# Kernel optimization log

Measured on AMD Instinct MI355X. Metric: run time of the kernel, lower is better.

Reference implementation:

```python
import jax, jax.numpy as jnp
import numpy as np

N_NODES = 20000
N_EDGES = 160000
MUL0, MUL1 = 32, 16          # 32x0e + 16x1o for both in and out irreps
EDGE_FEAT = 128
HIDDEN = 128
W_SIZES = [MUL0*MUL0, MUL1*MUL0, MUL0*MUL1, MUL1*MUL1, MUL1*MUL1]  # uvw weights per path (sh muls are 1)
W_OFF = np.cumsum([0] + W_SIZES).tolist()
W_NUMEL = W_OFF[-1]          # 2560
EPS_LN = 1e-5

_e = np.zeros((3, 3, 3), np.float32)
for i, j, k in [(0, 1, 2), (1, 2, 0), (2, 0, 1)]:
    _e[i, j, k] = 1.0
    _e[i, k, j] = -1.0
EPS3 = jnp.asarray(_e)  # Levi-Civita for 1o x 1o -> 1o path


def setup_inputs() -> dict:
    key = jax.random.key(0)
    ks = jax.random.split(key, 8)
    node_attr = jax.random.normal(ks[0], (N_NODES, MUL0 + 3 * MUL1), jnp.float32)
    edge_index = jax.random.randint(ks[1], (2, N_EDGES), 0, N_NODES)
    edge_attr = jax.random.normal(ks[2], (N_EDGES, EDGE_FEAT), jnp.float32)
    edge_sh = jax.random.normal(ks[3], (N_EDGES, 4), jnp.float32)
    s1 = float(1.0 / np.sqrt(EDGE_FEAT))
    s2 = float(1.0 / np.sqrt(HIDDEN))
    fc_w1 = jax.random.uniform(ks[4], (EDGE_FEAT, HIDDEN), jnp.float32, -s1, s1)
    fc_b1 = jnp.zeros((HIDDEN,), jnp.float32)
    fc_w2 = jax.random.uniform(ks[5], (HIDDEN, W_NUMEL), jnp.float32, -s2, s2)
    fc_b2 = jnp.zeros((W_NUMEL,), jnp.float32)
    # LayerNorm params: mean_shift is ones for scalar (0e) irreps, zeros for 1o
    mean_shift = jnp.concatenate(
        [jnp.ones((1, MUL0, 1), jnp.float32), jnp.zeros((1, MUL1, 1), jnp.float32)], axis=1)
    affine_weight = jnp.ones((MUL0 + MUL1,), jnp.float32) + 0.1 * jax.random.normal(ks[6], (MUL0 + MUL1,), jnp.float32)
    affine_bias = 0.02 * jax.random.normal(ks[7], (MUL0,), jnp.float32)
    return dict(node_attr=node_attr, edge_attr=edge_attr, edge_sh=edge_sh,
                fc_w1=fc_w1, fc_b1=fc_b1, fc_w2=fc_w2, fc_b2=fc_b2,
                mean_shift=mean_shift, affine_weight=affine_weight,
                affine_bias=affine_bias, edge_index=edge_index)


def _forward(node_attr, edge_attr, edge_sh, fc_w1, fc_b1, fc_w2, fc_b2,
             mean_shift, affine_weight, affine_bias, edge_index):
    edge_src, edge_dst = edge_index[0], edge_index[1]
    # gather source-of-message node features per edge
    x = node_attr[edge_dst]                          # [E, 80]
    x0 = x[:, :MUL0]                                 # [E, 32]   l=0 scalars
    x1 = x[:, MUL0:].reshape(-1, MUL1, 3)            # [E, 16, 3] l=1 vectors
    sh0 = edge_sh[:, 0]                              # [E]
    sh1 = edge_sh[:, 1:4]                            # [E, 3]

    # per-edge TP weights from edge features (SimpleLinear: Lin-ReLU-Lin, dropout=0)
    w = jnp.maximum(edge_attr @ fc_w1 + fc_b1, 0.0) @ fc_w2 + fc_b2   # [E, 2560]
    w1 = w[:, W_OFF[0]:W_OFF[1]].reshape(-1, MUL0, MUL0)
    w2 = w[:, W_OFF[1]:W_OFF[2]].reshape(-1, MUL1, MUL0)
    w3 = w[:, W_OFF[2]:W_OFF[3]].reshape(-1, MUL0, MUL1)
    w4 = w[:, W_OFF[3]:W_OFF[4]].reshape(-1, MUL1, MUL1)
    w5 = w[:, W_OFF[4]:W_OFF[5]].reshape(-1, MUL1, MUL1)

    # e3nn FullyConnectedTensorProduct normalization (component + element):
    # coeff = sqrt(ir_out.dim / sum_of_fan_in_over_paths_to_that_output)
    c0 = float(np.sqrt(1.0 / (MUL0 + MUL1)))            # -> 0e: fan 32+16
    c1 = float(np.sqrt(3.0 / (MUL0 + MUL1 + MUL1)))     # -> 1o: fan 32+16+16
    is3 = float(1.0 / np.sqrt(3.0))  # wigner-3j (110),(011),(101)
    is6 = float(1.0 / np.sqrt(6.0))  # wigner-3j (111)

    out0 = c0 * (jnp.einsum('eu,e,euw->ew', x0, sh0, w1)
                 + is3 * jnp.einsum('eui,ei,euw->ew', x1, sh1, w2))            # [E, 32]
    out1 = c1 * (is3 * jnp.einsum('eu,ek,euw->ewk', x0, sh1, w3)
                 + is3 * jnp.einsum('eui,e,euw->ewi', x1, sh0, w4)
                 + is6 * jnp.einsum('ijk,eui,ej,euw->ewk', EPS3, x1, sh1, w5)) # [E, 16, 3]
    tp = jnp.concatenate([out0, out1.reshape(-1, MUL1 * 3)], axis=-1)          # [E, 80]

    # scatter-mean over destination (edge_src) nodes
    seg = jax.ops.segment_sum(tp, edge_src, num_segments=N_NODES)
    cnt = jax.ops.segment_sum(jnp.ones((tp.shape[0],), tp.dtype), edge_src, num_segments=N_NODES)
    out = seg / jnp.maximum(cnt, 1.0)[:, None]

    # residual (out irreps == in irreps, so F.pad is a no-op)
    out = out + node_attr

    # equivariant LayerNorm (normalization='component')
    f0 = out[:, :MUL0].reshape(-1, MUL0, 1)
    f0 = f0 - jnp.mean(f0, axis=1, keepdims=True) * mean_shift[:, :MUL0]
    n0 = jnp.mean(jnp.mean(f0 * f0, axis=-1), axis=1, keepdims=True)           # [N, 1]
    n0 = jax.lax.rsqrt(n0 + EPS_LN) * affine_weight[None, :MUL0]               # [N, 32]
    f0 = f0 * n0[:, :, None] + affine_bias[None, :, None]

    f1 = out[:, MUL0:].reshape(-1, MUL1, 3)
    f1 = f1 - jnp.mean(f1, axis=1, keepdims=True) * mean_shift[:, MUL0:]       # mean_shift=0 here
    n1 = jnp.mean(jnp.mean(f1 * f1, axis=-1), axis=1, keepdims=True)
    n1 = jax.lax.rsqrt(n1 + EPS_LN) * affine_weight[None, MUL0:]
    f1 = f1 * n1[:, :, None]

    return jnp.concatenate([f0.reshape(-1, MUL0), f1.reshape(-1, MUL1 * 3)], axis=-1)


def reference(node_attr, edge_attr, edge_sh, fc_w1, fc_b1, fc_w2, fc_b2,
              mean_shift, affine_weight, affine_bias, edge_index):
    return _forward(node_attr, edge_attr, edge_sh, fc_w1, fc_b1, fc_w2, fc_b2,
                    mean_shift, affine_weight, affine_bias, edge_index)
```

## Files before the change

### kernel.cpp

```cpp
#include <hip/hip_runtime.h>

typedef __attribute__((ext_vector_type(8))) short short8;
typedef __attribute__((ext_vector_type(4))) short bfx4;
typedef __attribute__((ext_vector_type(4))) float floatx4;

#define N_NODES 20000
#define N_EDGES 160000
#define TILE_E 128
#define EBLK (N_EDGES / TILE_E)

#define C0f   0.14433756729740643f
#define C1f   0.21650635094610965f
#define IS3   0.5773502691896258f
#define IS6   0.4082482904638631f
#define EPS_LN 1e-5f

#define W1F_OFF 0
#define W2F_OFF 32768
#define CNT_OFF 688128

__device__ __forceinline__ short f2bf(float f) {
    unsigned u = __float_as_uint(f);
    u += 0x7fff + ((u >> 16) & 1);
    return (short)(u >> 16);
}
__device__ __forceinline__ float bf2f(short s) {
    return __uint_as_float(((unsigned)(unsigned short)s) << 16);
}

__device__ __forceinline__ short8 load8_bf16(const float* p) {
    const float4* q = (const float4*)p;
    float4 f0 = q[0], f1 = q[1];
    short8 s;
    s[0]=f2bf(f0.x); s[1]=f2bf(f0.y); s[2]=f2bf(f0.z); s[3]=f2bf(f0.w);
    s[4]=f2bf(f1.x); s[5]=f2bf(f1.y); s[6]=f2bf(f1.z); s[7]=f2bf(f1.w);
    return s;
}

__device__ __forceinline__ floatx4 mfma4(const short8* a, short8 b0, short8 b1,
                                         short8 b2, short8 b3, float bias) {
    floatx4 C = {bias, bias, bias, bias};
    C = __builtin_amdgcn_mfma_f32_16x16x32_bf16(a[0], b0, C, 0, 0, 0);
    C = __builtin_amdgcn_mfma_f32_16x16x32_bf16(a[1], b1, C, 0, 0, 0);
    C = __builtin_amdgcn_mfma_f32_16x16x32_bf16(a[2], b2, C, 0, 0, 0);
    C = __builtin_amdgcn_mfma_f32_16x16x32_bf16(a[3], b3, C, 0, 0, 0);
    return C;
}

__device__ __forceinline__ int xsw(int row, int el) {
    return row * 64 + ((el & 3) | ((((el >> 2) ^ row) & 15) << 2));
}
__device__ __forceinline__ bfx4 ldx(const short* base, int row, int gran) {
    return *(const bfx4*)(base + row * 64 + (((gran ^ row) & 15) << 2));
}

__global__ __launch_bounds__(256)
void prep_kernel(const float* __restrict__ fc_w1, const float* __restrict__ fc_w2,
                 short* __restrict__ w1f, short* __restrict__ w2f,
                 float* __restrict__ cnt) {
    int g = blockIdx.x * 256 + threadIdx.x;
    if (g < N_NODES) cnt[g] = 0.0f;
    if (g < 2048) {
        int ln = g & 15, qd = (g >> 4) & 3, kt = (g >> 6) & 3, t = g >> 8;
        int n = t * 16 + ln, kb = kt * 32 + qd * 8;
        short8 s;
        #pragma unroll
        for (int j = 0; j < 8; ++j) s[j] = f2bf(fc_w1[(kb + j) * 128 + n]);
        *(short8*)(w1f + g * 8) = s;
        return;
    }
    int g2 = g - 2048;
    if (g2 < 40960) {
        int ln = g2 & 15, qd = (g2 >> 4) & 3, kt = (g2 >> 6) & 3, t = g2 >> 8;
        int n = t * 16 + ln, kb = kt * 32 + qd * 8;
        short8 s;
        #pragma unroll
        for (int j = 0; j < 8; ++j) s[j] = f2bf(fc_w2[(kb + j) * 2560 + n]);
        int p = (t < 128) ? t : (t < 144 ? 128 + 2 * (t - 128) : 129 + 2 * (t - 144));
        *(short8*)(w2f + (size_t)p * 2048 + (g2 & 255) * 8) = s;
    }
}

__global__ __launch_bounds__(256, 2)
void edge_kernel(const float* __restrict__ node_attr,
                 const float* __restrict__ edge_attr,
                 const float* __restrict__ edge_sh,
                 const float* __restrict__ fc_b1,
                 const float* __restrict__ fc_b2,
                 const int*   __restrict__ edge_index,
                 const short* __restrict__ w1f,
                 const short* __restrict__ w2f,
                 float* __restrict__ accum,
                 float* __restrict__ cnt)
{
    __shared__ __align__(16) short s_pool[128 * 136];
    __shared__ __align__(16) short s_w2[2 * 8192];
    __shared__ float s_sh[128 * 4];
    __shared__ int   s_src[128];
    __shared__ int   s_dst[128];

    short* s_H    = s_pool;
    short* s_x0t  = s_pool;
    short* s_x1t  = s_pool + 4096;
    short* s_x1dt = s_pool + 10240;

    const int tid  = threadIdx.x;
    const int e0   = blockIdx.x * TILE_E;
    const int lane = tid & 63;
    const int wv   = tid >> 6;

    float4 st0, st1, st2, st3;
    {
        const float4* sp = (const float4*)w2f;
        st0 = sp[tid]; st1 = sp[tid + 256]; st2 = sp[tid + 512]; st3 = sp[tid + 768];
    }

    if (tid < 128) {
        int s = edge_index[e0 + tid];
        int d = edge_index[N_EDGES + e0 + tid];
        s_src[tid] = s; s_dst[tid] = d;
        atomicAdd(&cnt[s], 1.0f);
    }
    s_sh[tid]       = edge_sh[(size_t)e0 * 4 + tid];
    s_sh[tid + 256] = edge_sh[(size_t)e0 * 4 + tid + 256];
    __syncthreads();

    const int ln   = lane & 15;
    const int qd   = lane >> 4;
    const int eb0  = wv * 32 + qd * 4;
    const int eb1  = eb0 + 16;
    const int half = wv >> 1;
    const int gr0  = (wv & 1) * 8 + qd;
    const int gr1  = gr0 + 4;
    const short* x0b  = s_x0t  + half * 2048;
    const short* x1b  = s_x1t  + half * 3072;
    const short* x1db = s_x1dt + half * 1024;

    {
        short8 a1[2][4];
        #pragma unroll
        for (int g = 0; g < 2; ++g) {
            const float* ap = edge_attr + (size_t)(e0 + wv*32 + g*16 + ln) * 128 + qd * 8;
            #pragma unroll
            for (int kt = 0; kt < 4; ++kt) a1[g][kt] = load8_bf16(ap + kt * 32);
        }
        #pragma unroll
        for (int t = 0; t < 8; ++t) {
            const short* bp = w1f + t * 2048 + lane * 8;
            short8 b0 = *(const short8*)bp;
            short8 b1 = *(const short8*)(bp + 512);
            short8 b2 = *(const short8*)(bp + 1024);
            short8 b3 = *(const short8*)(bp + 1536);
            float bias = fc_b1[t * 16 + ln];
            #pragma unroll
            for (int g = 0; g < 2; ++g) {
                floatx4 C = mfma4(a1[g], b0, b1, b2, b3, bias);
                #pragma unroll
                for (int r = 0; r < 4; ++r)
                    s_H[(wv*32 + g*16 + qd*4 + r) * 136 + t*16 + ln] = f2bf(fmaxf(C[r], 0.f));
            }
        }
    }

    short8 a2[2][4];
    #pragma unroll
    for (int g = 0; g < 2; ++g) {
        const short* hp = s_H + (wv*32 + g*16 + ln) * 136 + qd * 8;
        #pragma unroll
        for (int kt = 0; kt < 4; ++kt) a2[g][kt] = *(const short8*)(hp + kt * 32);
    }
    __syncthreads();

    #pragma unroll
    for (int i = 0; i < 40; ++i) {
        int f = tid + i * 256;
        int e = f / 80, c = f % 80;
        float v = node_attr[(size_t)s_dst[e] * 80 + c];
        int hf = e >> 6, el = e & 63;
        if (c < 32) s_x0t[hf * 2048 + xsw(c, el)] = f2bf(v);
        else        s_x1t[hf * 3072 + xsw(c - 32, el)] = f2bf(v);
    }
    #pragma unroll
    for (int i = 0; i < 8; ++i) {
        int it = tid + i * 256;
        int e = it >> 4, u = it & 15;
        const float* xp = node_attr + (size_t)s_dst[e] * 80 + 32 + u * 3;
        float d = xp[0] * s_sh[e*4+1] + xp[1] * s_sh[e*4+2] + xp[2] * s_sh[e*4+3];
        s_x1dt[(e >> 6) * 1024 + xsw(u, e & 63)] = f2bf(d);
    }
    __syncthreads();

    {
        float4* dp = (float4*)s_w2;
        dp[tid] = st0; dp[tid+256] = st1; dp[tid+512] = st2; dp[tid+768] = st3;
        const float4* sp = (const float4*)(w2f + (size_t)8192);
        st0 = sp[tid]; st1 = sp[tid+256]; st2 = sp[tid+512]; st3 = sp[tid+768];
    }
    __syncthreads();


    float r0lo[2][4] = {}, r0hi[2][4] = {}, r1lo[2][4] = {}, r1hi[2][4] = {};

    #pragma unroll 1
    for (int c = 0; c < 16; ++c) {
        {
            float4* dp = (float4*)(s_w2 + ((c + 1) & 1) * 8192);
            dp[tid] = st0; dp[tid+256] = st1; dp[tid+512] = st2; dp[tid+768] = st3;
            const float4* sp = (const float4*)(w2f + (size_t)(c + 2) * 8192);
            st0 = sp[tid]; st1 = sp[tid+256]; st2 = sp[tid+512]; st3 = sp[tid+768];
        }
        const short* bb = s_w2 + (c & 1) * 8192 + lane * 8;
        #pragma unroll
        for (int t = 0; t < 2; ++t) {
            const int u = 2 * c + t;
            const short* bp = bb + t * 4096;
            short8 L0 = *(const short8*)bp,          L1 = *(const short8*)(bp + 512);
            short8 L2 = *(const short8*)(bp + 1024), L3 = *(const short8*)(bp + 1536);
            short8 H0 = *(const short8*)(bp + 2048), H1 = *(const short8*)(bp + 2560);
            short8 H2 = *(const short8*)(bp + 3072), H3 = *(const short8*)(bp + 3584);
            float blo = fc_b2[u * 32 + ln], bhi = fc_b2[u * 32 + 16 + ln];
            #pragma unroll
            for (int g = 0; g < 2; ++g) {
                floatx4 Clo = mfma4(a2[g], L0, L1, L2, L3, blo);
                floatx4 Chi = mfma4(a2[g], H0, H1, H2, H3, bhi);
                bfx4 xs = ldx(x0b, u, g ? gr1 : gr0);
                #pragma unroll
                for (int r = 0; r < 4; ++r) {
                    float a = bf2f(xs[r]);
                    r0lo[g][r] += a * Clo[r];
                    r0hi[g][r] += a * Chi[r];
                }
            }
        }
        __syncthreads();
    }
    #pragma unroll 1
    for (int c2 = 0; c2 < 8; ++c2) {
        const int c = 16 + c2;
        {
            float4* dp = (float4*)(s_w2 + ((c + 1) & 1) * 8192);
            dp[tid] = st0; dp[tid+256] = st1; dp[tid+512] = st2; dp[tid+768] = st3;
            const float4* sp = (const float4*)(w2f + (size_t)(c + 2) * 8192);
            st0 = sp[tid]; st1 = sp[tid+256]; st2 = sp[tid+512]; st3 = sp[tid+768];
        }
        const short* bb = s_w2 + (c & 1) * 8192 + lane * 8;
        #pragma unroll
        for (int t = 0; t < 2; ++t) {
            const int u = 2 * c2 + t;
            const short* bp = bb + t * 4096;
            short8 L0 = *(const short8*)bp,          L1 = *(const short8*)(bp + 512);
            short8 L2 = *(const short8*)(bp + 1024), L3 = *(const short8*)(bp + 1536);
            short8 H0 = *(const short8*)(bp + 2048), H1 = *(const short8*)(bp + 2560);
            short8 H2 = *(const short8*)(bp + 3072), H3 = *(const short8*)(bp + 3584);
            float blo = fc_b2[1024 + u * 32 + ln], bhi = fc_b2[1024 + u * 32 + 16 + ln];
            #pragma unroll
            for (int g = 0; g < 2; ++g) {
                floatx4 Clo = mfma4(a2[g], L0, L1, L2, L3, blo);
                floatx4 Chi = mfma4(a2[g], H0, H1, H2, H3, bhi);
                bfx4 xs = ldx(x1db, u, g ? gr1 : gr0);
                #pragma unroll
                for (int r = 0; r < 4; ++r) {
                    float a = bf2f(xs[r]);
                    r1lo[g][r] += a * Clo[r];
                    r1hi[g][r] += a * Chi[r];
                }
            }
        }
        __syncthreads();
    }
    #pragma unroll
    for (int g = 0; g < 2; ++g)
        #pragma unroll
        for (int r = 0; r < 4; ++r) {
            int e = (g ? eb1 : eb0) + r;
            float sh0 = s_sh[e*4];
            int base = s_src[e] * 80;
            atomicAdd(&accum[base + ln],      C0f * (sh0 * r0lo[g][r] + IS3 * r1lo[g][r]));
            atomicAdd(&accum[base + 16 + ln], C0f * (sh0 * r0hi[g][r] + IS3 * r1hi[g][r]));
        }

    float r3[2][4] = {};
    float r4[2][4][3] = {};
    float r5[2][4][3] = {};

    #pragma unroll 1
    for (int c3 = 0; c3 < 8; ++c3) {
        const int c = 24 + c3;
        {
            float4* dp = (float4*)(s_w2 + ((c + 1) & 1) * 8192);
            dp[tid] = st0; dp[tid+256] = st1; dp[tid+512] = st2; dp[tid+768] = st3;
            const float4* sp = (const float4*)(w2f + (size_t)(c + 2) * 8192);
            st0 = sp[tid]; st1 = sp[tid+256]; st2 = sp[tid+512]; st3 = sp[tid+768];
        }
        const short* bb = s_w2 + (c & 1) * 8192 + lane * 8;
        #pragma unroll
        for (int t = 0; t < 4; ++t) {
            const int u = 4 * c3 + t;
            const short* bp = bb + t * 2048;
            short8 b0 = *(const short8*)bp,          b1 = *(const short8*)(bp + 512);
            short8 b2 = *(const short8*)(bp + 1024), b3 = *(const short8*)(bp + 1536);
            float bias = fc_b2[1536 + u * 16 + ln];
            #pragma unroll
            for (int g = 0; g < 2; ++g) {
                floatx4 C = mfma4(a2[g], b0, b1, b2, b3, bias);
                bfx4 xs = ldx(x0b, u, g ? gr1 : gr0);
                #pragma unroll
                for (int r = 0; r < 4; ++r)
                    r3[g][r] += bf2f(xs[r]) * C[r];
            }
        }
        __syncthreads();
    }
    #pragma unroll 1
    for (int c4 = 0; c4 < 8; ++c4) {
        const int c = 32 + c4;
        if (c4 < 7) {
            float4* dp = (float4*)(s_w2 + ((c + 1) & 1) * 8192);
            dp[tid] = st0; dp[tid+256] = st1; dp[tid+512] = st2; dp[tid+768] = st3;
            if (c4 < 6) {
                const float4* sp = (const float4*)(w2f + (size_t)(c + 2) * 8192);
                st0 = sp[tid]; st1 = sp[tid+256]; st2 = sp[tid+512]; st3 = sp[tid+768];
            }
        }
        const short* bb = s_w2 + (c & 1) * 8192 + lane * 8;
        #pragma unroll
        for (int t = 0; t < 2; ++t) {
            const int u = 2 * c4 + t;
            const short* bpF = bb + (2 * t) * 2048;
            short8 F0 = *(const short8*)bpF,          F1 = *(const short8*)(bpF + 512);
            short8 F2 = *(const short8*)(bpF + 1024), F3 = *(const short8*)(bpF + 1536);
            short8 G0 = *(const short8*)(bpF + 2048), G1 = *(const short8*)(bpF + 2560);
            short8 G2 = *(const short8*)(bpF + 3072), G3 = *(const short8*)(bpF + 3584);
            float b4 = fc_b2[2048 + u * 16 + ln], b5 = fc_b2[2304 + u * 16 + ln];
            #pragma unroll
            for (int g = 0; g < 2; ++g) {
                floatx4 C4 = mfma4(a2[g], F0, F1, F2, F3, b4);
                floatx4 C5 = mfma4(a2[g], G0, G1, G2, G3, b5);
                int gr = (g ? gr1 : gr0);
                bfx4 x0s = ldx(x1b, u*3 + 0, gr);
                bfx4 x1s = ldx(x1b, u*3 + 1, gr);
                bfx4 x2s = ldx(x1b, u*3 + 2, gr);
                #pragma unroll
                for (int r = 0; r < 4; ++r) {
                    float a0 = bf2f(x0s[r]), a1 = bf2f(x1s[r]), a2v = bf2f(x2s[r]);
                    r4[g][r][0] += a0 * C4[r];  r5[g][r][0] += a0 * C5[r];
                    r4[g][r][1] += a1 * C4[r];  r5[g][r][1] += a1 * C5[r];
                    r4[g][r][2] += a2v * C4[r]; r5[g][r][2] += a2v * C5[r];
                }
            }
        }
        if (c4 < 7) __syncthreads();
    }
    #pragma unroll
    for (int g = 0; g < 2; ++g)
        #pragma unroll
        for (int r = 0; r < 4; ++r) {
            int e = (g ? eb1 : eb0) + r;
            float sh0 = s_sh[e*4], sa = s_sh[e*4+1], sb = s_sh[e*4+2], sc = s_sh[e*4+3];
            int base = s_src[e] * 80;
            float t3 = C1f * IS3 * r3[g][r];
            float s0 = C1f * IS3 * sh0;
            float c6 = C1f * IS6;
            float v50 = r5[g][r][1] * sc - r5[g][r][2] * sb;
            float v51 = r5[g][r][2] * sa - r5[g][r][0] * sc;
            float v52 = r5[g][r][0] * sb - r5[g][r][1] * sa;
            atomicAdd(&accum[base + 32 + ln*3 + 0], sa * t3 + s0 * r4[g][r][0] + c6 * v50);
            atomicAdd(&accum[base + 32 + ln*3 + 1], sb * t3 + s0 * r4[g][r][1] + c6 * v51);
            atomicAdd(&accum[base + 32 + ln*3 + 2], sc * t3 + s0 * r4[g][r][2] + c6 * v52);
        }
}

__global__ __launch_bounds__(256)
void node_kernel(const float* __restrict__ node_attr,
                 const float* __restrict__ mean_shift,
                 const float* __restrict__ aw,
                 const float* __restrict__ ab,
                 const float* __restrict__ cnt,
                 float* __restrict__ out)
{
    __shared__ float sv[64 * 85];
    __shared__ float s_inv[64];
    const int tid = threadIdx.x;
    const int n0  = blockIdx.x * 64;

    if (tid < 64) {
        int n = n0 + tid;
        s_inv[tid] = (n < N_NODES) ? 1.0f / fmaxf(cnt[n], 1.0f) : 0.0f;
    }
    __syncthreads();

    #pragma unroll
    for (int i = 0; i < 20; ++i) {
        int idx = tid + i * 256;
        int r = idx / 80, cch = idx % 80;
        int n = n0 + r;
        if (n < N_NODES) {
            float o = out[(size_t)n * 80 + cch];
            float a = node_attr[(size_t)n * 80 + cch];
            sv[r * 85 + cch] = o * s_inv[r] + a;
        }
    }
    __syncthreads();

    if (tid < 64 && n0 + tid < N_NODES) {
        float v[80];
        const float* sp = sv + tid * 85;
        #pragma unroll
        for (int k = 0; k < 80; ++k) v[k] = sp[k];

        float m0 = 0.f;
        #pragma unroll
        for (int u = 0; u < 32; ++u) m0 += v[u];
        m0 *= (1.0f / 32.0f);
        float n0v = 0.f;
        #pragma unroll
        for (int u = 0; u < 32; ++u) {
            float f = v[u] - m0 * mean_shift[u];
            v[u] = f;
            n0v += f * f;
        }
        n0v = rsqrtf(n0v * (1.0f / 32.0f) + EPS_LN);
        #pragma unroll
        for (int u = 0; u < 32; ++u) v[u] = v[u] * (n0v * aw[u]) + ab[u];

        float m1[3] = {0.f, 0.f, 0.f};
        #pragma unroll
        for (int u = 0; u < 16; ++u)
            #pragma unroll
            for (int i = 0; i < 3; ++i) m1[i] += v[32 + u*3 + i];
        #pragma unroll
        for (int i = 0; i < 3; ++i) m1[i] *= (1.0f / 16.0f);
        float n1 = 0.f;
        #pragma unroll
        for (int u = 0; u < 16; ++u)
            #pragma unroll
            for (int i = 0; i < 3; ++i) {
                float f = v[32 + u*3 + i] - m1[i] * mean_shift[32 + u];
                v[32 + u*3 + i] = f;
                n1 += f * f;
            }
        n1 = rsqrtf(n1 * (1.0f / 48.0f) + EPS_LN);
        #pragma unroll
        for (int u = 0; u < 16; ++u)
            #pragma unroll
            for (int i = 0; i < 3; ++i)
                v[32 + u*3 + i] *= (n1 * aw[32 + u]);

        float* wp = sv + tid * 85;
        #pragma unroll
        for (int k = 0; k < 80; ++k) wp[k] = v[k];
    }
    __syncthreads();

    #pragma unroll
    for (int i = 0; i < 20; ++i) {
        int idx = tid + i * 256;
        int r = idx / 80, cch = idx % 80;
        int n = n0 + r;
        if (n < N_NODES) out[(size_t)n * 80 + cch] = sv[r * 85 + cch];
    }
}

extern "C" void kernel_launch(void* const* d_in, const int* in_sizes, int n_in,
                              void* d_out, int out_size, void* d_ws, size_t ws_size,
                              hipStream_t stream) {
    const float* node_attr  = (const float*)d_in[0];
    const float* edge_attr  = (const float*)d_in[1];
    const float* edge_sh    = (const float*)d_in[2];
    const float* fc_w1      = (const float*)d_in[3];
    const float* fc_b1      = (const float*)d_in[4];
    const float* fc_w2      = (const float*)d_in[5];
    const float* fc_b2      = (const float*)d_in[6];
    const float* mean_shift = (const float*)d_in[7];
    const float* aw         = (const float*)d_in[8];
    const float* ab         = (const float*)d_in[9];
    const int*   edge_index = (const int*)d_in[10];
    float* out = (float*)d_out;

    short* w1f = (short*)((char*)d_ws + W1F_OFF);
    short* w2f = (short*)((char*)d_ws + W2F_OFF);
    float* cnt = (float*)((char*)d_ws + CNT_OFF);

    (void)hipMemsetAsync(d_out, 0, (size_t)N_NODES * 80 * sizeof(float), stream);

    prep_kernel<<<(2048 + 40960 + 255) / 256, 256, 0, stream>>>(fc_w1, fc_w2, w1f, w2f, cnt);
    edge_kernel<<<EBLK, 256, 0, stream>>>(node_attr, edge_attr, edge_sh,
                                          fc_b1, fc_b2, edge_index,
                                          w1f, w2f, out, cnt);
    node_kernel<<<(N_NODES + 63) / 64, 256, 0, stream>>>(node_attr, mean_shift,
                                                         aw, ab, cnt, out);
}
```

Measured before the change: 336.4 us.

## Halve W2 staging chunks, swizzle hidden tile, fold output memset into prep

The double-buffered W2 staging now uses 8 KB chunks (80 steps) instead of 16 KB (40 steps). This halves the staging registers and the LDS W2 buffer. The hidden-activation tile drops its padding and uses an XOR swizzle to avoid bank conflicts, which shrinks LDS further. This is likely aimed at fitting more blocks per CU or easing register pressure. The output zeroing moves from a separate memset into the prep kernel, removing one launch, at the cost of twice as many block barriers in the edge kernel.

```diff
diff --git a/kernel.cpp b/kernel.cpp
--- a/kernel.cpp
+++ b/kernel.cpp
@@ -54,12 +54,18 @@
     return *(const bfx4*)(base + row * 64 + (((gran ^ row) & 15) << 2));
 }
 
+__device__ __forceinline__ int hsw(int row, int col) {
+    return row * 128 + (col & 7) + ((((col >> 3) ^ (row & 15)) & 15) << 3);
+}
+
 __global__ __launch_bounds__(256)
 void prep_kernel(const float* __restrict__ fc_w1, const float* __restrict__ fc_w2,
                  short* __restrict__ w1f, short* __restrict__ w2f,
-                 float* __restrict__ cnt) {
+                 float* __restrict__ cnt, float* __restrict__ out) {
     int g = blockIdx.x * 256 + threadIdx.x;
     if (g < N_NODES) cnt[g] = 0.0f;
+    float4 z = {0.f, 0.f, 0.f, 0.f};
+    for (int i = g; i < 400000; i += 43008) ((float4*)out)[i] = z;
     if (g < 2048) {
         int ln = g & 15, qd = (g >> 4) & 3, kt = (g >> 6) & 3, t = g >> 8;
         int n = t * 16 + ln, kb = kt * 32 + qd * 8;
@@ -67,17 +73,17 @@
         #pragma unroll
         for (int j = 0; j < 8; ++j) s[j] = f2bf(fc_w1[(kb + j) * 128 + n]);
         *(short8*)(w1f + g * 8) = s;
-        return;
-    }
-    int g2 = g - 2048;
-    if (g2 < 40960) {
-        int ln = g2 & 15, qd = (g2 >> 4) & 3, kt = (g2 >> 6) & 3, t = g2 >> 8;
-        int n = t * 16 + ln, kb = kt * 32 + qd * 8;
-        short8 s;
-        #pragma unroll
-        for (int j = 0; j < 8; ++j) s[j] = f2bf(fc_w2[(kb + j) * 2560 + n]);
-        int p = (t < 128) ? t : (t < 144 ? 128 + 2 * (t - 128) : 129 + 2 * (t - 144));
-        *(short8*)(w2f + (size_t)p * 2048 + (g2 & 255) * 8) = s;
+    } else {
+        int g2 = g - 2048;
+        if (g2 < 40960) {
+            int ln = g2 & 15, qd = (g2 >> 4) & 3, kt = (g2 >> 6) & 3, t = g2 >> 8;
+            int n = t * 16 + ln, kb = kt * 32 + qd * 8;
+            short8 s;
+            #pragma unroll
+            for (int j = 0; j < 8; ++j) s[j] = f2bf(fc_w2[(kb + j) * 2560 + n]);
+            int p = (t < 128) ? t : (t < 144 ? 128 + 2 * (t - 128) : 129 + 2 * (t - 144));
+            *(short8*)(w2f + (size_t)p * 2048 + (g2 & 255) * 8) = s;
+        }
     }
 }
 
@@ -93,8 +99,8 @@
                  float* __restrict__ accum,
                  float* __restrict__ cnt)
 {
-    __shared__ __align__(16) short s_pool[128 * 136];
-    __shared__ __align__(16) short s_w2[2 * 8192];
+    __shared__ __align__(16) short s_pool[128 * 128];
+    __shared__ __align__(16) short s_w2[2 * 4096];
     __shared__ float s_sh[128 * 4];
     __shared__ int   s_src[128];
     __shared__ int   s_dst[128];
@@ -109,10 +115,10 @@
     const int lane = tid & 63;
     const int wv   = tid >> 6;
 
-    float4 st0, st1, st2, st3;
+    float4 stA, stB;
     {
         const float4* sp = (const float4*)w2f;
-        st0 = sp[tid]; st1 = sp[tid + 256]; st2 = sp[tid + 512]; st3 = sp[tid + 768];
+        stA = sp[tid]; stB = sp[tid + 256];
     }
 
     if (tid < 128) {
@@ -157,7 +163,7 @@
                 floatx4 C = mfma4(a1[g], b0, b1, b2, b3, bias);
                 #pragma unroll
                 for (int r = 0; r < 4; ++r)
-                    s_H[(wv*32 + g*16 + qd*4 + r) * 136 + t*16 + ln] = f2bf(fmaxf(C[r], 0.f));
+                    s_H[hsw(wv*32 + g*16 + qd*4 + r, t*16 + ln)] = f2bf(fmaxf(C[r], 0.f));
             }
         }
     }
@@ -165,9 +171,11 @@
     short8 a2[2][4];
     #pragma unroll
     for (int g = 0; g < 2; ++g) {
-        const short* hp = s_H + (wv*32 + g*16 + ln) * 136 + qd * 8;
-        #pragma unroll
-        for (int kt = 0; kt < 4; ++kt) a2[g][kt] = *(const short8*)(hp + kt * 32);
+        const int row = wv*32 + g*16 + ln;
+        #pragma unroll
+        for (int kt = 0; kt < 4; ++kt)
+            a2[g][kt] = *(const short8*)(s_H + row * 128 +
+                                         (((qd + 4*kt) ^ (row & 15)) << 3));
     }
     __syncthreads();
 
@@ -188,82 +196,69 @@
         float d = xp[0] * s_sh[e*4+1] + xp[1] * s_sh[e*4+2] + xp[2] * s_sh[e*4+3];
         s_x1dt[(e >> 6) * 1024 + xsw(u, e & 63)] = f2bf(d);
     }
-    __syncthreads();
-
     {
         float4* dp = (float4*)s_w2;
-        dp[tid] = st0; dp[tid+256] = st1; dp[tid+512] = st2; dp[tid+768] = st3;
-        const float4* sp = (const float4*)(w2f + (size_t)8192);
-        st0 = sp[tid]; st1 = sp[tid+256]; st2 = sp[tid+512]; st3 = sp[tid+768];
-    }
-    __syncthreads();
-
+        dp[tid] = stA; dp[tid + 256] = stB;
+        const float4* sp = (const float4*)(w2f + 4096);
+        stA = sp[tid]; stB = sp[tid + 256];
+    }
+    __syncthreads();
+
+    auto stage_step = [&](int cg) {
+        if (cg + 1 < 80) {
+            float4* dp = (float4*)(s_w2 + ((cg + 1) & 1) * 4096);
+            dp[tid] = stA; dp[tid + 256] = stB;
+        }
+        if (cg + 2 < 80) {
+            const float4* sp = (const float4*)(w2f + (size_t)(cg + 2) * 4096);
+            stA = sp[tid]; stB = sp[tid + 256];
+        }
+    };
 
     float r0lo[2][4] = {}, r0hi[2][4] = {}, r1lo[2][4] = {}, r1hi[2][4] = {};
 
     #pragma unroll 1
-    for (int c = 0; c < 16; ++c) {
-        {
-            float4* dp = (float4*)(s_w2 + ((c + 1) & 1) * 8192);
-            dp[tid] = st0; dp[tid+256] = st1; dp[tid+512] = st2; dp[tid+768] = st3;
-            const float4* sp = (const float4*)(w2f + (size_t)(c + 2) * 8192);
-            st0 = sp[tid]; st1 = sp[tid+256]; st2 = sp[tid+512]; st3 = sp[tid+768];
-        }
-        const short* bb = s_w2 + (c & 1) * 8192 + lane * 8;
-        #pragma unroll
-        for (int t = 0; t < 2; ++t) {
-            const int u = 2 * c + t;
-            const short* bp = bb + t * 4096;
-            short8 L0 = *(const short8*)bp,          L1 = *(const short8*)(bp + 512);
-            short8 L2 = *(const short8*)(bp + 1024), L3 = *(const short8*)(bp + 1536);
-            short8 H0 = *(const short8*)(bp + 2048), H1 = *(const short8*)(bp + 2560);
-            short8 H2 = *(const short8*)(bp + 3072), H3 = *(const short8*)(bp + 3584);
-            float blo = fc_b2[u * 32 + ln], bhi = fc_b2[u * 32 + 16 + ln];
-            #pragma unroll
-            for (int g = 0; g < 2; ++g) {
-                floatx4 Clo = mfma4(a2[g], L0, L1, L2, L3, blo);
-                floatx4 Chi = mfma4(a2[g], H0, H1, H2, H3, bhi);
-                bfx4 xs = ldx(x0b, u, g ? gr1 : gr0);
-                #pragma unroll
-                for (int r = 0; r < 4; ++r) {
-                    float a = bf2f(xs[r]);
-                    r0lo[g][r] += a * Clo[r];
-                    r0hi[g][r] += a * Chi[r];
-                }
+    for (int c = 0; c < 32; ++c) {
+        stage_step(c);
+        const short* bp = s_w2 + (c & 1) * 4096 + lane * 8;
+        short8 L0 = *(const short8*)bp,          L1 = *(const short8*)(bp + 512);
+        short8 L2 = *(const short8*)(bp + 1024), L3 = *(const short8*)(bp + 1536);
+        short8 H0 = *(const short8*)(bp + 2048), H1 = *(const short8*)(bp + 2560);
+        short8 H2 = *(const short8*)(bp + 3072), H3 = *(const short8*)(bp + 3584);
+        float blo = fc_b2[c * 32 + ln], bhi = fc_b2[c * 32 + 16 + ln];
+        #pragma unroll
+        for (int g = 0; g < 2; ++g) {
+            floatx4 Clo = mfma4(a2[g], L0, L1, L2, L3, blo);
+            floatx4 Chi = mfma4(a2[g], H0, H1, H2, H3, bhi);
+            bfx4 xs = ldx(x0b, c, g ? gr1 : gr0);
+            #pragma unroll
+            for (int r = 0; r < 4; ++r) {
+                float a = bf2f(xs[r]);
+                r0lo[g][r] += a * Clo[r];
+                r0hi[g][r] += a * Chi[r];
             }
         }
         __syncthreads();
     }
     #pragma unroll 1
-    for (int c2 = 0; c2 < 8; ++c2) {
-        const int c = 16 + c2;
-        {
-            float4* dp = (float4*)(s_w2 + ((c + 1) & 1) * 8192);
-            dp[tid] = st0; dp[tid+256] = st1; dp[tid+512] = st2; dp[tid+768] = st3;
-            const float4* sp = (const float4*)(w2f + (size_t)(c + 2) * 8192);
-            st0 = sp[tid]; st1 = sp[tid+256]; st2 = sp[tid+512]; st3 = sp[tid+768];
-        }
-        const short* bb = s_w2 + (c & 1) * 8192 + lane * 8;
-        #pragma unroll
-        for (int t = 0; t < 2; ++t) {
-            const int u = 2 * c2 + t;
-            const short* bp = bb + t * 4096;
-            short8 L0 = *(const short8*)bp,          L1 = *(const short8*)(bp + 512);
-            short8 L2 = *(const short8*)(bp + 1024), L3 = *(const short8*)(bp + 1536);
-            short8 H0 = *(const short8*)(bp + 2048), H1 = *(const short8*)(bp + 2560);
-            short8 H2 = *(const short8*)(bp + 3072), H3 = *(const short8*)(bp + 3584);
-            float blo = fc_b2[1024 + u * 32 + ln], bhi = fc_b2[1024 + u * 32 + 16 + ln];
-            #pragma unroll
-            for (int g = 0; g < 2; ++g) {
-                floatx4 Clo = mfma4(a2[g], L0, L1, L2, L3, blo);
-                floatx4 Chi = mfma4(a2[g], H0, H1, H2, H3, bhi);
-                bfx4 xs = ldx(x1db, u, g ? gr1 : gr0);
-                #pragma unroll
-                for (int r = 0; r < 4; ++r) {
-                    float a = bf2f(xs[r]);
-                    r1lo[g][r] += a * Clo[r];
-                    r1hi[g][r] += a * Chi[r];
-                }
+    for (int c2 = 0; c2 < 16; ++c2) {
+        stage_step(32 + c2);
+        const short* bp = s_w2 + ((32 + c2) & 1) * 4096 + lane * 8;
+        short8 L0 = *(const short8*)bp,          L1 = *(const short8*)(bp + 512);
+        short8 L2 = *(const short8*)(bp + 1024), L3 = *(const short8*)(bp + 1536);
+        short8 H0 = *(const short8*)(bp + 2048), H1 = *(const short8*)(bp + 2560);
+        short8 H2 = *(const short8*)(bp + 3072), H3 = *(const short8*)(bp + 3584);
+        float blo = fc_b2[1024 + c2 * 32 + ln], bhi = fc_b2[1024 + c2 * 32 + 16 + ln];
+        #pragma unroll
+        for (int g = 0; g < 2; ++g) {
+            floatx4 Clo = mfma4(a2[g], L0, L1, L2, L3, blo);
+            floatx4 Chi = mfma4(a2[g], H0, H1, H2, H3, bhi);
+            bfx4 xs = ldx(x1db, c2, g ? gr1 : gr0);
+            #pragma unroll
+            for (int r = 0; r < 4; ++r) {
+                float a = bf2f(xs[r]);
+                r1lo[g][r] += a * Clo[r];
+                r1hi[g][r] += a * Chi[r];
             }
         }
         __syncthreads();
@@ -284,18 +279,12 @@
     float r5[2][4][3] = {};
 
     #pragma unroll 1
-    for (int c3 = 0; c3 < 8; ++c3) {
-        const int c = 24 + c3;
-        {
-            float4* dp = (float4*)(s_w2 + ((c + 1) & 1) * 8192);
-            dp[tid] = st0; dp[tid+256] = st1; dp[tid+512] = st2; dp[tid+768] = st3;
-            const float4* sp = (const float4*)(w2f + (size_t)(c + 2) * 8192);
-            st0 = sp[tid]; st1 = sp[tid+256]; st2 = sp[tid+512]; st3 = sp[tid+768];
-        }
-        const short* bb = s_w2 + (c & 1) * 8192 + lane * 8;
-        #pragma unroll
-        for (int t = 0; t < 4; ++t) {
-            const int u = 4 * c3 + t;
+    for (int c3 = 0; c3 < 16; ++c3) {
+        stage_step(48 + c3);
+        const short* bb = s_w2 + ((48 + c3) & 1) * 4096 + lane * 8;
+        #pragma unroll
+        for (int t = 0; t < 2; ++t) {
+            const int u = 2 * c3 + t;
             const short* bp = bb + t * 2048;
             short8 b0 = *(const short8*)bp,          b1 = *(const short8*)(bp + 512);
             short8 b2 = *(const short8*)(bp + 1024), b3 = *(const short8*)(bp + 1536);
@@ -312,44 +301,32 @@
         __syncthreads();
     }
     #pragma unroll 1
-    for (int c4 = 0; c4 < 8; ++c4) {
-        const int c = 32 + c4;
-        if (c4 < 7) {
-            float4* dp = (float4*)(s_w2 + ((c + 1) & 1) * 8192);
-            dp[tid] = st0; dp[tid+256] = st1; dp[tid+512] = st2; dp[tid+768] = st3;
-            if (c4 < 6) {
-                const float4* sp = (const float4*)(w2f + (size_t)(c + 2) * 8192);
-                st0 = sp[tid]; st1 = sp[tid+256]; st2 = sp[tid+512]; st3 = sp[tid+768];
-            }
-        }
-        const short* bb = s_w2 + (c & 1) * 8192 + lane * 8;
-        #pragma unroll
-        for (int t = 0; t < 2; ++t) {
-            const int u = 2 * c4 + t;
-            const short* bpF = bb + (2 * t) * 2048;
-            short8 F0 = *(const short8*)bpF,          F1 = *(const short8*)(bpF + 512);
-            short8 F2 = *(const short8*)(bpF + 1024), F3 = *(const short8*)(bpF + 1536);
-            short8 G0 = *(const short8*)(bpF + 2048), G1 = *(const short8*)(bpF + 2560);
-            short8 G2 = *(const short8*)(bpF + 3072), G3 = *(const short8*)(bpF + 3584);
-            float b4 = fc_b2[2048 + u * 16 + ln], b5 = fc_b2[2304 + u * 16 + ln];
-            #pragma unroll
-            for (int g = 0; g < 2; ++g) {
-                floatx4 C4 = mfma4(a2[g], F0, F1, F2, F3, b4);
-                floatx4 C5 = mfma4(a2[g], G0, G1, G2, G3, b5);
-                int gr = (g ? gr1 : gr0);
-                bfx4 x0s = ldx(x1b, u*3 + 0, gr);
-                bfx4 x1s = ldx(x1b, u*3 + 1, gr);
-                bfx4 x2s = ldx(x1b, u*3 + 2, gr);
-                #pragma unroll
-                for (int r = 0; r < 4; ++r) {
-                    float a0 = bf2f(x0s[r]), a1 = bf2f(x1s[r]), a2v = bf2f(x2s[r]);
-                    r4[g][r][0] += a0 * C4[r];  r5[g][r][0] += a0 * C5[r];
-                    r4[g][r][1] += a1 * C4[r];  r5[g][r][1] += a1 * C5[r];
-                    r4[g][r][2] += a2v * C4[r]; r5[g][r][2] += a2v * C5[r];
-                }
-            }
-        }
-        if (c4 < 7) __syncthreads();
+    for (int c4 = 0; c4 < 16; ++c4) {
+        const int cg = 64 + c4;
+        stage_step(cg);
+        const short* bb = s_w2 + (cg & 1) * 4096 + lane * 8;
+        short8 F0 = *(const short8*)bb,          F1 = *(const short8*)(bb + 512);
+        short8 F2 = *(const short8*)(bb + 1024), F3 = *(const short8*)(bb + 1536);
+        short8 G0 = *(const short8*)(bb + 2048), G1 = *(const short8*)(bb + 2560);
+        short8 G2 = *(const short8*)(bb + 3072), G3 = *(const short8*)(bb + 3584);
+        float b4 = fc_b2[2048 + c4 * 16 + ln], b5 = fc_b2[2304 + c4 * 16 + ln];
+        #pragma unroll
+        for (int g = 0; g < 2; ++g) {
+            floatx4 C4 = mfma4(a2[g], F0, F1, F2, F3, b4);
+            floatx4 C5 = mfma4(a2[g], G0, G1, G2, G3, b5);
+            int gr = (g ? gr1 : gr0);
+            bfx4 x0s = ldx(x1b, c4*3 + 0, gr);
+            bfx4 x1s = ldx(x1b, c4*3 + 1, gr);
+            bfx4 x2s = ldx(x1b, c4*3 + 2, gr);
+            #pragma unroll
+            for (int r = 0; r < 4; ++r) {
+                float a0 = bf2f(x0s[r]), a1 = bf2f(x1s[r]), a2v = bf2f(x2s[r]);
+                r4[g][r][0] += a0 * C4[r];  r5[g][r][0] += a0 * C5[r];
+                r4[g][r][1] += a1 * C4[r];  r5[g][r][1] += a1 * C5[r];
+                r4[g][r][2] += a2v * C4[r]; r5[g][r][2] += a2v * C5[r];
+            }
+        }
+        if (c4 < 15) __syncthreads();
     }
     #pragma unroll
     for (int g = 0; g < 2; ++g)
@@ -481,9 +458,8 @@
     short* w2f = (short*)((char*)d_ws + W2F_OFF);
     float* cnt = (float*)((char*)d_ws + CNT_OFF);
 
-    (void)hipMemsetAsync(d_out, 0, (size_t)N_NODES * 80 * sizeof(float), stream);
-
-    prep_kernel<<<(2048 + 40960 + 255) / 256, 256, 0, stream>>>(fc_w1, fc_w2, w1f, w2f, cnt);
+    prep_kernel<<<(2048 + 40960 + 255) / 256, 256, 0, stream>>>(fc_w1, fc_w2, w1f, w2f,
+                                                                cnt, out);
     edge_kernel<<<EBLK, 256, 0, stream>>>(node_attr, edge_attr, edge_sh,
                                           fc_b1, fc_b2, edge_index,
                                           w1f, w2f, out, cnt);
```

Measured after the change: 363.3 us. 1.08x slower.

## Replace float atomic scatter with CSR-bucketed per-edge writes and node-side gather

Applied to the files above, without the earlier changes.

Source-node degrees are counted in the prep kernel, then a single-block scan kernel builds per-node offsets. Each edge claims a slot with one integer atomic and writes its 80 message values to a slot-ordered buffer with plain stores instead of 80 float atomics. The node kernel then sums each node's contiguous slots before LayerNorm, which removes the memset of the output. This trades atomic contention for an extra ~51MB write and read pass, a serial single-block scan, and a workspace requirement that is not checked.

```diff
diff --git a/kernel.cpp b/kernel.cpp
--- a/kernel.cpp
+++ b/kernel.cpp
@@ -15,9 +15,13 @@
 #define IS6   0.4082482904638631f
 #define EPS_LN 1e-5f
 
-#define W1F_OFF 0
-#define W2F_OFF 32768
-#define CNT_OFF 688128
+#define W1F_OFF  0
+#define W2F_OFF  32768
+#define CNT_OFF  688128
+#define OFF_OFF  768128
+#define FILL_OFF 848128
+#define TP_OFF   1048576
+#define WS_NEED  (TP_OFF + (size_t)N_EDGES * 80 * 4)
 
 __device__ __forceinline__ short f2bf(float f) {
     unsigned u = __float_as_uint(f);
@@ -57,9 +61,13 @@
 __global__ __launch_bounds__(256)
 void prep_kernel(const float* __restrict__ fc_w1, const float* __restrict__ fc_w2,
                  short* __restrict__ w1f, short* __restrict__ w2f,
-                 float* __restrict__ cnt) {
+                 int* __restrict__ cnt, const int* __restrict__ edge_index,
+                 int do_count) {
     int g = blockIdx.x * 256 + threadIdx.x;
-    if (g < N_NODES) cnt[g] = 0.0f;
+    if (do_count) {
+        for (int e = g; e < N_EDGES; e += 43008)
+            atomicAdd(&cnt[edge_index[e]], 1);
+    }
     if (g < 2048) {
         int ln = g & 15, qd = (g >> 4) & 3, kt = (g >> 6) & 3, t = g >> 8;
         int n = t * 16 + ln, kb = kt * 32 + qd * 8;
@@ -67,17 +75,48 @@
         #pragma unroll
         for (int j = 0; j < 8; ++j) s[j] = f2bf(fc_w1[(kb + j) * 128 + n]);
         *(short8*)(w1f + g * 8) = s;
-        return;
-    }
-    int g2 = g - 2048;
-    if (g2 < 40960) {
-        int ln = g2 & 15, qd = (g2 >> 4) & 3, kt = (g2 >> 6) & 3, t = g2 >> 8;
-        int n = t * 16 + ln, kb = kt * 32 + qd * 8;
-        short8 s;
-        #pragma unroll
-        for (int j = 0; j < 8; ++j) s[j] = f2bf(fc_w2[(kb + j) * 2560 + n]);
-        int p = (t < 128) ? t : (t < 144 ? 128 + 2 * (t - 128) : 129 + 2 * (t - 144));
-        *(short8*)(w2f + (size_t)p * 2048 + (g2 & 255) * 8) = s;
+    } else {
+        int g2 = g - 2048;
+        if (g2 < 40960) {
+            int ln = g2 & 15, qd = (g2 >> 4) & 3, kt = (g2 >> 6) & 3, t = g2 >> 8;
+            int n = t * 16 + ln, kb = kt * 32 + qd * 8;
+            short8 s;
+            #pragma unroll
+            for (int j = 0; j < 8; ++j) s[j] = f2bf(fc_w2[(kb + j) * 2560 + n]);
+            int p = (t < 128) ? t : (t < 144 ? 128 + 2 * (t - 128) : 129 + 2 * (t - 144));
+            *(short8*)(w2f + (size_t)p * 2048 + (g2 & 255) * 8) = s;
+        }
+    }
+}
+
+__global__ __launch_bounds__(1024)
+void scan_kernel(const int* __restrict__ cnt, int* __restrict__ off,
+                 int* __restrict__ fill) {
+    __shared__ int part[1024];
+    const int t = threadIdx.x;
+    const int base = t * 20;
+    int loc[20];
+    int s = 0;
+    if (base < N_NODES) {
+        #pragma unroll
+        for (int i = 0; i < 20; ++i) { loc[i] = s; s += cnt[base + i]; }
+    }
+    part[t] = s;
+    __syncthreads();
+    for (int d = 1; d < 1024; d <<= 1) {
+        int v = (t >= d) ? part[t - d] : 0;
+        __syncthreads();
+        part[t] += v;
+        __syncthreads();
+    }
+    int pre = (t == 0) ? 0 : part[t - 1];
+    if (base < N_NODES) {
+        #pragma unroll
+        for (int i = 0; i < 20; ++i) {
+            int o = pre + loc[i];
+            off[base + i] = o;
+            fill[base + i] = o;
+        }
     }
 }
 
@@ -90,13 +129,13 @@
                  const int*   __restrict__ edge_index,
                  const short* __restrict__ w1f,
                  const short* __restrict__ w2f,
-                 float* __restrict__ accum,
-                 float* __restrict__ cnt)
+                 int*   __restrict__ fill,
+                 float* __restrict__ tp)
 {
     __shared__ __align__(16) short s_pool[128 * 136];
     __shared__ __align__(16) short s_w2[2 * 8192];
     __shared__ float s_sh[128 * 4];
-    __shared__ int   s_src[128];
+    __shared__ int   s_slot[128];
     __shared__ int   s_dst[128];
 
     short* s_H    = s_pool;
@@ -118,8 +157,8 @@
     if (tid < 128) {
         int s = edge_index[e0 + tid];
         int d = edge_index[N_EDGES + e0 + tid];
-        s_src[tid] = s; s_dst[tid] = d;
-        atomicAdd(&cnt[s], 1.0f);
+        s_slot[tid] = atomicAdd(&fill[s], 1);
+        s_dst[tid] = d;
     }
     s_sh[tid]       = edge_sh[(size_t)e0 * 4 + tid];
     s_sh[tid + 256] = edge_sh[(size_t)e0 * 4 + tid + 256];
@@ -274,9 +313,9 @@
         for (int r = 0; r < 4; ++r) {
             int e = (g ? eb1 : eb0) + r;
             float sh0 = s_sh[e*4];
-            int base = s_src[e] * 80;
-            atomicAdd(&accum[base + ln],      C0f * (sh0 * r0lo[g][r] + IS3 * r1lo[g][r]));
-            atomicAdd(&accum[base + 16 + ln], C0f * (sh0 * r0hi[g][r] + IS3 * r1hi[g][r]));
+            float* tpe = tp + (size_t)s_slot[e] * 80;
+            tpe[ln]      = C0f * (sh0 * r0lo[g][r] + IS3 * r1lo[g][r]);
+            tpe[16 + ln] = C0f * (sh0 * r0hi[g][r] + IS3 * r1hi[g][r]);
         }
 
     float r3[2][4] = {};
@@ -357,16 +396,16 @@
         for (int r = 0; r < 4; ++r) {
             int e = (g ? eb1 : eb0) + r;
             float sh0 = s_sh[e*4], sa = s_sh[e*4+1], sb = s_sh[e*4+2], sc = s_sh[e*4+3];
-            int base = s_src[e] * 80;
+            float* tpe = tp + (size_t)s_slot[e] * 80;
             float t3 = C1f * IS3 * r3[g][r];
             float s0 = C1f * IS3 * sh0;
             float c6 = C1f * IS6;
             float v50 = r5[g][r][1] * sc - r5[g][r][2] * sb;
             float v51 = r5[g][r][2] * sa - r5[g][r][0] * sc;
             float v52 = r5[g][r][0] * sb - r5[g][r][1] * sa;
-            atomicAdd(&accum[base + 32 + ln*3 + 0], sa * t3 + s0 * r4[g][r][0] + c6 * v50);
-            atomicAdd(&accum[base + 32 + ln*3 + 1], sb * t3 + s0 * r4[g][r][1] + c6 * v51);
-            atomicAdd(&accum[base + 32 + ln*3 + 2], sc * t3 + s0 * r4[g][r][2] + c6 * v52);
+            tpe[32 + ln*3 + 0] = sa * t3 + s0 * r4[g][r][0] + c6 * v50;
+            tpe[32 + ln*3 + 1] = sb * t3 + s0 * r4[g][r][1] + c6 * v51;
+            tpe[32 + ln*3 + 2] = sc * t3 + s0 * r4[g][r][2] + c6 * v52;
         }
 }
 
@@ -375,29 +414,49 @@
                  const float* __restrict__ mean_shift,
                  const float* __restrict__ aw,
                  const float* __restrict__ ab,
-                 const float* __restrict__ cnt,
+                 const int* __restrict__ cnt,
+                 const int* __restrict__ off,
+                 const float* __restrict__ tp,
                  float* __restrict__ out)
 {
     __shared__ float sv[64 * 85];
-    __shared__ float s_inv[64];
+    __shared__ int s_off[64], s_cnt[64];
     const int tid = threadIdx.x;
     const int n0  = blockIdx.x * 64;
 
     if (tid < 64) {
         int n = n0 + tid;
-        s_inv[tid] = (n < N_NODES) ? 1.0f / fmaxf(cnt[n], 1.0f) : 0.0f;
-    }
-    __syncthreads();
-
-    #pragma unroll
-    for (int i = 0; i < 20; ++i) {
-        int idx = tid + i * 256;
-        int r = idx / 80, cch = idx % 80;
+        s_off[tid] = (n < N_NODES) ? off[n] : 0;
+        s_cnt[tid] = (n < N_NODES) ? cnt[n] : 0;
+    }
+    __syncthreads();
+
+    {
+        int r = tid >> 2, q = tid & 3;
         int n = n0 + r;
         if (n < N_NODES) {
-            float o = out[(size_t)n * 80 + cch];
-            float a = node_attr[(size_t)n * 80 + cch];
-            sv[r * 85 + cch] = o * s_inv[r] + a;
+            int o = s_off[r], kc = s_cnt[r];
+            float acc[20] = {};
+            for (int k = 0; k < kc; ++k) {
+                const float4* p = (const float4*)(tp + (size_t)(o + k) * 80 + q * 20);
+                #pragma unroll
+                for (int j = 0; j < 5; ++j) {
+                    float4 v = p[j];
+                    acc[4*j+0] += v.x; acc[4*j+1] += v.y;
+                    acc[4*j+2] += v.z; acc[4*j+3] += v.w;
+                }
+            }
+            float inv = 1.0f / fmaxf((float)kc, 1.0f);
+            const float4* a4 = (const float4*)(node_attr + (size_t)n * 80 + q * 20);
+            float* sp = sv + r * 85 + q * 20;
+            #pragma unroll
+            for (int j = 0; j < 5; ++j) {
+                float4 a = a4[j];
+                sp[4*j+0] = acc[4*j+0] * inv + a.x;
+                sp[4*j+1] = acc[4*j+1] * inv + a.y;
+                sp[4*j+2] = acc[4*j+2] * inv + a.z;
+                sp[4*j+3] = acc[4*j+3] * inv + a.w;
+            }
         }
     }
     __syncthreads();
@@ -477,16 +536,21 @@
     const int*   edge_index = (const int*)d_in[10];
     float* out = (float*)d_out;
 
-    short* w1f = (short*)((char*)d_ws + W1F_OFF);
-    short* w2f = (short*)((char*)d_ws + W2F_OFF);
-    float* cnt = (float*)((char*)d_ws + CNT_OFF);
-
-    (void)hipMemsetAsync(d_out, 0, (size_t)N_NODES * 80 * sizeof(float), stream);
-
-    prep_kernel<<<(2048 + 40960 + 255) / 256, 256, 0, stream>>>(fc_w1, fc_w2, w1f, w2f, cnt);
+    short* w1f  = (short*)((char*)d_ws + W1F_OFF);
+    short* w2f  = (short*)((char*)d_ws + W2F_OFF);
+    int*   cnt  = (int*)((char*)d_ws + CNT_OFF);
+    int*   off  = (int*)((char*)d_ws + OFF_OFF);
+    int*   fill = (int*)((char*)d_ws + FILL_OFF);
+    float* tp   = (float*)((char*)d_ws + TP_OFF);
+
+    (void)hipMemsetAsync(cnt, 0, N_NODES * sizeof(int), stream);
+
+    prep_kernel<<<(2048 + 40960 + 255) / 256, 256, 0, stream>>>(
+        fc_w1, fc_w2, w1f, w2f, cnt, edge_index, 1);
+    scan_kernel<<<1, 1024, 0, stream>>>(cnt, off, fill);
     edge_kernel<<<EBLK, 256, 0, stream>>>(node_attr, edge_attr, edge_sh,
                                           fc_b1, fc_b2, edge_index,
-                                          w1f, w2f, out, cnt);
+                                          w1f, w2f, fill, tp);
     node_kernel<<<(N_NODES + 63) / 64, 256, 0, stream>>>(node_attr, mean_shift,
-                                                         aw, ab, cnt, out);
-}
+                                                         aw, ab, cnt, off, tp, out);
+}
```

Measured after the change: 308.5 us. 8.3% less time.
